# Kernel optimization log

Hardware: AMD Instinct MI355X
Metric: run time of the kernel (lower is better)

The kernel has to match this reference:

```python
import jax, jax.numpy as jnp
import numpy as np

NUM_HEADS = 8
NUM_GROUPS = 32
EPS = 1e-5


def setup_inputs() -> dict:
    key = jax.random.key(0)
    ks = jax.random.split(key, 7)
    B, C, H, W = 8, 512, 32, 32
    x = jax.random.normal(ks[0], (B, C, H, W), dtype=jnp.float32)
    # GroupNorm affine params
    gn_w = jnp.ones((C,), dtype=jnp.float32)
    gn_b = jnp.zeros((C,), dtype=jnp.float32)
    # 1x1 conv == linear over channel dim; store squeezed weights (out, in)
    qkv_w = jax.random.normal(ks[1], (3 * C, C), dtype=jnp.float32) * (1.0 / np.sqrt(C))
    qkv_b = jnp.zeros((3 * C,), dtype=jnp.float32)
    proj_w = jax.random.normal(ks[2], (C, C), dtype=jnp.float32) * (1.0 / np.sqrt(C))
    proj_b = jnp.zeros((C,), dtype=jnp.float32)
    return {"x": x, "gn_w": gn_w, "gn_b": gn_b, "qkv_w": qkv_w,
            "qkv_b": qkv_b, "proj_w": proj_w, "proj_b": proj_b}


def reference(x, gn_w, gn_b, qkv_w, qkv_b, proj_w, proj_b):
    B, C, H, W = x.shape
    G = NUM_GROUPS
    hd = C // NUM_HEADS
    scale = hd ** -0.5
    # GroupNorm: normalize over (C//G, H, W) per group
    xg = x.reshape(B, G, C // G, H, W)
    mean = xg.mean(axis=(2, 3, 4), keepdims=True)
    var = xg.var(axis=(2, 3, 4), keepdims=True)
    xn = ((xg - mean) * jax.lax.rsqrt(var + EPS)).reshape(B, C, H, W)
    xn = xn * gn_w[None, :, None, None] + gn_b[None, :, None, None]
    # QKV 1x1 conv
    qkv = jnp.einsum('bchw,oc->bohw', xn, qkv_w) + qkv_b[None, :, None, None]
    # (B, 3, heads, head_dim, HW) -> (3, B, heads, HW, head_dim)
    qkv = qkv.reshape(B, 3, NUM_HEADS, hd, H * W).transpose(1, 0, 2, 4, 3)
    q, k, v = qkv[0], qkv[1], qkv[2]
    attn = jax.nn.softmax(jnp.einsum('bhqd,bhkd->bhqk', q, k) * scale, axis=-1)
    out = jnp.einsum('bhqk,bhkd->bhqd', attn, v)  # (B, heads, HW, hd)
    out = out.transpose(0, 1, 3, 2).reshape(B, C, H, W)
    out = jnp.einsum('bchw,oc->bohw', out, proj_w) + proj_b[None, :, None, None]
    return out + x
```

## Files before the change

kernel.cpp:

```cpp
#include <hip/hip_runtime.h>
#include <hip/hip_bf16.h>
#include <math.h>

typedef __bf16 bf16_t;
typedef __bf16 bf16x8 __attribute__((ext_vector_type(8)));
typedef __bf16 bf16x4 __attribute__((ext_vector_type(4)));
typedef float  f32x4  __attribute__((ext_vector_type(4)));
typedef short  short4v __attribute__((ext_vector_type(4)));

#define NB    8
#define NC    512
#define NHW   1024
#define NHEAD 8
#define NHD   64
#define NG    32
#define NCG   16
#define NO3   1536
#define KVB   64
#define NKT   16

__device__ __forceinline__ void lds_load16(bf16_t* lds, const bf16_t* g) {
  __builtin_amdgcn_global_load_lds(
      (__attribute__((address_space(1))) unsigned int*)(g),
      (__attribute__((address_space(3))) unsigned int*)(void*)(lds),
      16, 0, 0);
}

__device__ __forceinline__ f32x4 mfma16(bf16x4 a, bf16x4 b, f32x4 c) {
#if __has_builtin(__builtin_amdgcn_mfma_f32_16x16x16bf16_1k)
  return __builtin_amdgcn_mfma_f32_16x16x16bf16_1k(
      __builtin_bit_cast(short4v, a), __builtin_bit_cast(short4v, b), c, 0, 0, 0);
#else
  f32x4 d;
  asm("v_mfma_f32_16x16x16_bf16 %0, %1, %2, %3"
      : "=v"(d) : "v"(a), "v"(b), "v"(c));
  return d;
#endif
}

__global__ __launch_bounds__(256)
void gn_kernel(const float* __restrict__ x, const float* __restrict__ gw,
               const float* __restrict__ gb, bf16_t* __restrict__ xn)
{
  const int bg = blockIdx.x;
  const int b = bg >> 5, g = bg & 31;
  const float* xp = x + ((size_t)b * NC + g * NCG) * NHW;
  const int tid = threadIdx.x;
  const int wave = tid >> 6, lane = tid & 63;

  float s1 = 0.f, s2 = 0.f;
  const float4* xp4 = (const float4*)xp;
  for (int i = tid; i < 4096; i += 256) {
    float4 v = xp4[i];
    s1 += v.x + v.y + v.z + v.w;
    s2 += v.x * v.x + v.y * v.y + v.z * v.z + v.w * v.w;
  }
  for (int off = 32; off > 0; off >>= 1) {
    s1 += __shfl_down(s1, off);
    s2 += __shfl_down(s2, off);
  }
  __shared__ float red[16];
  if (lane == 0) { red[wave] = s1; red[8 + wave] = s2; }
  __syncthreads();
  float tot1 = red[0] + red[1] + red[2] + red[3];
  float tot2 = red[8] + red[9] + red[10] + red[11];
  const float mean = tot1 * (1.0f / 16384.0f);
  const float var  = tot2 * (1.0f / 16384.0f) - mean * mean;
  const float rstd = rsqrtf(var + 1e-5f);

  float gam[NCG], bet[NCG];
  #pragma unroll
  for (int c = 0; c < NCG; ++c) {
    gam[c] = gw[g * NCG + c] * rstd;
    bet[c] = gb[g * NCG + c] - mean * gam[c];
  }
  bf16_t* op = xn + (size_t)b * NHW * NC + g * NCG;
  for (int s = tid; s < NHW; s += 256) {
    __align__(16) bf16_t vals[NCG];
    #pragma unroll
    for (int c = 0; c < NCG; ++c)
      vals[c] = (bf16_t)(xp[c * NHW + s] * gam[c] + bet[c]);
    *(bf16x8*)(op + (size_t)s * NC)     = *(const bf16x8*)&vals[0];
    *(bf16x8*)(op + (size_t)s * NC + 8) = *(const bf16x8*)&vals[8];
  }
}

__global__ __launch_bounds__(256)
void wconv_kernel(const float* __restrict__ qw, const float* __restrict__ pw,
                  bf16_t* __restrict__ qwb, bf16_t* __restrict__ pwb)
{
  const int gid = blockIdx.x * 256 + threadIdx.x;
  const int n1 = NO3 * NC / 4;
  float4 v; bf16x4 o;
  if (gid < n1) {
    v = ((const float4*)qw)[gid];
    o[0] = (bf16_t)v.x; o[1] = (bf16_t)v.y; o[2] = (bf16_t)v.z; o[3] = (bf16_t)v.w;
    ((bf16x4*)qwb)[gid] = o;
  } else {
    int g2 = gid - n1;
    v = ((const float4*)pw)[g2];
    o[0] = (bf16_t)v.x; o[1] = (bf16_t)v.y; o[2] = (bf16_t)v.z; o[3] = (bf16_t)v.w;
    ((bf16x4*)pwb)[g2] = o;
  }
}

__device__ __forceinline__ void gemm_mainloop(const bf16_t* Ap, const bf16_t* Bp,
                                              bf16_t* sA, bf16_t* sB, f32x4 (&acc)[4][4])
{
  const int tid = threadIdx.x;
  const int wave = tid >> 6, lane = tid & 63;
  const int quad = lane >> 4, l16 = lane & 15;
  const int wm = wave >> 1, wn = wave & 1;
  for (int k0 = 0; k0 < 512; k0 += 32) {
    #pragma unroll
    for (int j = 0; j < 2; ++j) {
      int c = wave * 64 + j * 256 + lane;
      int row = c >> 2, ko = (c & 3) * 8;
      lds_load16(sA + (size_t)(wave * 64 + j * 256) * 8, Ap + (size_t)row * 512 + k0 + ko);
      lds_load16(sB + (size_t)(wave * 64 + j * 256) * 8, Bp + (size_t)row * 512 + k0 + ko);
    }
    __syncthreads();
    bf16x8 af[4], bfr[4];
    #pragma unroll
    for (int mi = 0; mi < 4; ++mi)
      af[mi] = *(const bf16x8*)(sA + (wm * 64 + mi * 16 + l16) * 32 + quad * 8);
    #pragma unroll
    for (int ni = 0; ni < 4; ++ni)
      bfr[ni] = *(const bf16x8*)(sB + (wn * 64 + ni * 16 + l16) * 32 + quad * 8);
    #pragma unroll
    for (int mi = 0; mi < 4; ++mi)
      #pragma unroll
      for (int ni = 0; ni < 4; ++ni)
        acc[mi][ni] = __builtin_amdgcn_mfma_f32_16x16x32_bf16(af[mi], bfr[ni], acc[mi][ni], 0, 0, 0);
    __syncthreads();
  }
}

__global__ __launch_bounds__(256, 2)
void qkv_gemm(const bf16_t* __restrict__ xn, const bf16_t* __restrict__ w,
              const float* __restrict__ bias,
              bf16_t* __restrict__ qbuf, bf16_t* __restrict__ kbuf, bf16_t* __restrict__ vbuf)
{
  __shared__ __align__(16) bf16_t smem[128 * 136];
  bf16_t* sA = smem;
  bf16_t* sB = smem + 4096;
  const int tid = threadIdx.x;
  const int wave = tid >> 6, lane = tid & 63;
  const int quad = lane >> 4, l16 = lane & 15;
  const int wm = wave >> 1, wn = wave & 1;
  const int bx = blockIdx.x, by = blockIdx.y, b = blockIdx.z;

  const bf16_t* Ap = xn + ((size_t)b * NHW + by * 128) * NC;
  const bf16_t* Bp = w + (size_t)bx * 128 * NC;
  f32x4 acc[4][4] = {};
  gemm_mainloop(Ap, Bp, sA, sB, acc);

  const int obase = bx * 128 + wn * 64;
  const int sbase = by * 128 + wm * 64;
  float bv[4];
  #pragma unroll
  for (int ni = 0; ni < 4; ++ni) bv[ni] = bias[obase + ni * 16 + l16];

  if (bx < 8) {
    const bool isq = (bx < 4);
    bf16_t* basep = isq ? qbuf : kbuf;
    const float scale = isq ? 0.18033688f : 1.0f;
    #pragma unroll
    for (int ni = 0; ni < 4; ++ni) {
      int o = obase + ni * 16 + l16;
      int hh = (o >> 6) & 7, dd = o & 63;
      bf16_t* dst = basep + ((size_t)(b * NHEAD + hh) * NHW) * NHD + dd;
      #pragma unroll
      for (int mi = 0; mi < 4; ++mi)
        #pragma unroll
        for (int r = 0; r < 4; ++r) {
          int s = sbase + mi * 16 + quad * 4 + r;
          dst[(size_t)s * NHD] = (bf16_t)((acc[mi][ni][r] + bv[ni]) * scale);
        }
    }
  } else {
    bf16_t* sC = smem;
    __syncthreads();
    #pragma unroll
    for (int ni = 0; ni < 4; ++ni)
      #pragma unroll
      for (int mi = 0; mi < 4; ++mi)
        #pragma unroll
        for (int r = 0; r < 4; ++r)
          sC[(wn * 64 + ni * 16 + l16) * 136 + wm * 64 + mi * 16 + quad * 4 + r] =
              (bf16_t)(acc[mi][ni][r] + bv[ni]);
    __syncthreads();
    int o_local = tid >> 1, shalf = (tid & 1) << 6;
    int ov = (bx - 8) * 128 + o_local;
    int hh = ov >> 6, dd = ov & 63;
    bf16_t* dst = vbuf + ((size_t)(b * NHEAD + hh) * NHD + dd) * NHW + by * 128 + shalf;
    #pragma unroll
    for (int jj = 0; jj < 8; ++jj)
      *(bf16x8*)(dst + jj * 8) = *(const bf16x8*)&sC[o_local * 136 + shalf + jj * 8];
  }
}

__global__ __launch_bounds__(256, 2)
void attn_kernel(const bf16_t* __restrict__ qbuf, const bf16_t* __restrict__ kbuf,
                 const bf16_t* __restrict__ vbuf, bf16_t* __restrict__ obuf)
{
  __shared__ __align__(16) char smem[32768];
  f32x4* mO = (f32x4*)smem;
  float* mM = (float*)(smem + 16384);
  float* mL = (float*)(smem + 17408);

  const int tid = threadIdx.x;
  const int wave = tid >> 6, lane = tid & 63;
  const int quad = lane >> 4, l16 = lane & 15;
  const int wl = wave & 1;
  const int wg = wave >> 1;
  const int idx = blockIdx.x;
  const int qt = idx >> 6, h = (idx >> 3) & 7, b = idx & 7;
  const size_t bh = (size_t)b * NHEAD + h;
  const bf16_t* qp = qbuf + (bh * NHW + qt * 64 + wl * 32) * NHD;
  const char* kp = (const char*)(kbuf + bh * NHW * NHD);
  const char* vp = (const char*)(vbuf + bh * NHD * NHW);

  const int r8 = lane >> 3;
  const int swc = (((lane & 7) << 4)) ^ (r8 << 4);

  bf16x8 qf[2][2];
  #pragma unroll
  for (int stile = 0; stile < 2; ++stile)
    #pragma unroll
    for (int kc = 0; kc < 2; ++kc)
      qf[stile][kc] = *(const bf16x8*)(qp + (size_t)(stile * 16 + l16) * NHD + kc * 32 + quad * 8);

  float m_i[2] = {-1e30f, -1e30f};
  float ll[2] = {0.f, 0.f};
  f32x4 oacc[4][2] = {};

  #pragma unroll
  for (int j = 0; j < 2; ++j) {
    int i = wave * 2 + j;
    const char* kg = kp + ((size_t)(i * 8 + r8) * NHD) * 2 + swc;
    lds_load16((bf16_t*)(smem + i * 1024), (const bf16_t*)kg);
    const char* vg = vp + ((size_t)(i * 8 + r8) * NHW) * 2 + swc;
    lds_load16((bf16_t*)(smem + 8192 + i * 1024), (const bf16_t*)vg);
  }
  __syncthreads();

  const int swr = (l16 & 7) << 4;

  for (int kt = 0; kt < NKT; ++kt) {
    const int cur = kt & 1;
    const char* Kb = smem + cur * 16384;
    const char* Vb = Kb + 8192;
    if (kt < NKT - 1) {
      char* Kn = smem + (cur ^ 1) * 16384;
      #pragma unroll
      for (int j = 0; j < 2; ++j) {
        int i = wave * 2 + j;
        const char* kg = kp + ((size_t)((kt + 1) * KVB + i * 8 + r8) * NHD) * 2 + swc;
        lds_load16((bf16_t*)(Kn + i * 1024), (const bf16_t*)kg);
        const char* vg = vp + ((size_t)(i * 8 + r8) * NHW + (kt + 1) * KVB) * 2 + swc;
        lds_load16((bf16_t*)(Kn + 8192 + i * 1024), (const bf16_t*)vg);
      }
    }

    f32x4 st[2][2];
    __builtin_amdgcn_s_setprio(1);
    #pragma unroll
    for (int mt = 0; mt < 2; ++mt) {
      const int mtg = wg * 2 + mt;
      const char* krow = Kb + (mtg * 16 + l16) * 128;
      bf16x8 ka0 = *(const bf16x8*)(krow + ((quad * 16) ^ swr));
      bf16x8 ka1 = *(const bf16x8*)(krow + ((64 + quad * 16) ^ swr));
      #pragma unroll
      for (int stile = 0; stile < 2; ++stile) {
        f32x4 z = {};
        z = __builtin_amdgcn_mfma_f32_16x16x32_bf16(ka0, qf[stile][0], z, 0, 0, 0);
        z = __builtin_amdgcn_mfma_f32_16x16x32_bf16(ka1, qf[stile][1], z, 0, 0, 0);
        st[stile][mt] = z;
      }
    }
    __builtin_amdgcn_s_setprio(0);

    #pragma unroll
    for (int stile = 0; stile < 2; ++stile) {
      float mx = st[stile][0][0];
      #pragma unroll
      for (int mt = 0; mt < 2; ++mt)
        #pragma unroll
        for (int r = 0; r < 4; ++r) mx = fmaxf(mx, st[stile][mt][r]);
      if (!__all(mx <= m_i[stile])) {
        mx = fmaxf(mx, __shfl_xor(mx, 16));
        mx = fmaxf(mx, __shfl_xor(mx, 32));
        float mnew = fmaxf(m_i[stile], mx);
        float alpha = exp2f(m_i[stile] - mnew);
        m_i[stile] = mnew;
        ll[stile] *= alpha;
        #pragma unroll
        for (int mi = 0; mi < 4; ++mi)
          #pragma unroll
          for (int r = 0; r < 4; ++r) oacc[mi][stile][r] *= alpha;
      }
      float rs = 0.f;
      #pragma unroll
      for (int mt = 0; mt < 2; ++mt)
        #pragma unroll
        for (int r = 0; r < 4; ++r) {
          float p = exp2f(st[stile][mt][r] - m_i[stile]);
          rs += p;
          st[stile][mt][r] = p;
        }
      ll[stile] += rs;
    }

    __builtin_amdgcn_s_setprio(1);
    #pragma unroll
    for (int mt = 0; mt < 2; ++mt) {
      const int mtg = wg * 2 + mt;
      bf16x4 pb[2];
      #pragma unroll
      for (int stile = 0; stile < 2; ++stile) {
        pb[stile][0] = (bf16_t)st[stile][mt][0];
        pb[stile][1] = (bf16_t)st[stile][mt][1];
        pb[stile][2] = (bf16_t)st[stile][mt][2];
        pb[stile][3] = (bf16_t)st[stile][mt][3];
      }
      #pragma unroll
      for (int mi = 0; mi < 4; ++mi) {
        const char* vrow = Vb + (mi * 16 + l16) * 128;
        bf16x4 va = *(const bf16x4*)(vrow + ((mtg * 32 + quad * 8) ^ swr));
        oacc[mi][0] = mfma16(va, pb[0], oacc[mi][0]);
        oacc[mi][1] = mfma16(va, pb[1], oacc[mi][1]);
      }
    }
    __builtin_amdgcn_s_setprio(0);
    __syncthreads();
  }

  float l_i[2];
  #pragma unroll
  for (int stile = 0; stile < 2; ++stile) {
    float rs = ll[stile];
    rs += __shfl_xor(rs, 16);
    rs += __shfl_xor(rs, 32);
    l_i[stile] = rs;
  }

  if (wg == 1) {
    #pragma unroll
    for (int stile = 0; stile < 2; ++stile) {
      mM[(wl * 2 + stile) * 64 + lane] = m_i[stile];
      mL[(wl * 2 + stile) * 64 + lane] = l_i[stile];
      #pragma unroll
      for (int mi = 0; mi < 4; ++mi)
        mO[((wl * 2 + stile) * 4 + mi) * 64 + lane] = oacc[mi][stile];
    }
  }
  __syncthreads();
  if (wg == 0) {
    #pragma unroll
    for (int stile = 0; stile < 2; ++stile) {
      float mB = mM[(wl * 2 + stile) * 64 + lane];
      float lB = mL[(wl * 2 + stile) * 64 + lane];
      float mS = fmaxf(m_i[stile], mB);
      float aA = exp2f(m_i[stile] - mS);
      float aB = exp2f(mB - mS);
      float inv = 1.0f / (l_i[stile] * aA + lB * aB);
      int s = qt * 64 + wl * 32 + stile * 16 + l16;
      bf16_t* orow = obuf + ((size_t)b * NHW + s) * NC + h * NHD;
      #pragma unroll
      for (int mi = 0; mi < 4; ++mi) {
        f32x4 oB = mO[((wl * 2 + stile) * 4 + mi) * 64 + lane];
        __align__(8) bf16_t o4[4];
        #pragma unroll
        for (int r = 0; r < 4; ++r)
          o4[r] = (bf16_t)((oacc[mi][stile][r] * aA + oB[r] * aB) * inv);
        *(bf16x4*)(orow + mi * 16 + quad * 4) = *(const bf16x4*)o4;
      }
    }
  }
}

__global__ __launch_bounds__(256, 2)
void proj_gemm(const bf16_t* __restrict__ ob, const bf16_t* __restrict__ w,
               const float* __restrict__ bias, const float* __restrict__ x,
               float* __restrict__ out)
{
  __shared__ __align__(16) bf16_t smem[8192];
  bf16_t* sA = smem;
  bf16_t* sB = smem + 4096;
  const int tid = threadIdx.x;
  const int wave = tid >> 6, lane = tid & 63;
  const int quad = lane >> 4, l16 = lane & 15;
  const int wm = wave >> 1, wn = wave & 1;
  const int bx = blockIdx.x, by = blockIdx.y, b = blockIdx.z;

  const bf16_t* Ap = w + (size_t)by * 128 * NC;
  const bf16_t* Bp = ob + ((size_t)b * NHW + bx * 128) * NC;
  f32x4 acc[4][4] = {};
  gemm_mainloop(Ap, Bp, sA, sB, acc);

  const int cobase = by * 128 + wm * 64;
  const int sbase  = bx * 128 + wn * 64;
  #pragma unroll
  for (int mi = 0; mi < 4; ++mi)
    #pragma unroll
    for (int r = 0; r < 4; ++r) {
      int co = cobase + mi * 16 + quad * 4 + r;
      float pb = bias[co];
      const float* xrow = x + ((size_t)b * NC + co) * NHW;
      float* orow = out + ((size_t)b * NC + co) * NHW;
      #pragma unroll
      for (int ni = 0; ni < 4; ++ni) {
        int s = sbase + ni * 16 + l16;
        orow[s] = acc[mi][ni][r] + pb + xrow[s];
      }
    }
}

extern "C" void kernel_launch(void* const* d_in, const int* in_sizes, int n_in,
                              void* d_out, int out_size, void* d_ws, size_t ws_size,
                              hipStream_t stream)
{
  const float* x      = (const float*)d_in[0];
  const float* gn_w   = (const float*)d_in[1];
  const float* gn_b   = (const float*)d_in[2];
  const float* qkv_w  = (const float*)d_in[3];
  const float* qkv_b  = (const float*)d_in[4];
  const float* proj_w = (const float*)d_in[5];
  const float* proj_b = (const float*)d_in[6];
  float* out = (float*)d_out;

  char* ws = (char*)d_ws;
  bf16_t* xn   = (bf16_t*)(ws);
  bf16_t* qwb  = (bf16_t*)(ws + 8388608);
  bf16_t* pwb  = (bf16_t*)(ws + 9961472);
  bf16_t* qbuf = (bf16_t*)(ws + 10485760);
  bf16_t* kbuf = (bf16_t*)(ws + 18874368);
  bf16_t* vbuf = (bf16_t*)(ws + 27262976);
  bf16_t* obuf = xn;

  gn_kernel<<<dim3(NB * NG), dim3(256), 0, stream>>>(x, gn_w, gn_b, xn);
  wconv_kernel<<<dim3(1024), dim3(256), 0, stream>>>(qkv_w, proj_w, qwb, pwb);
  qkv_gemm<<<dim3(12, 8, NB), dim3(256), 0, stream>>>(xn, qwb, qkv_b, qbuf, kbuf, vbuf);
  attn_kernel<<<dim3(1024), dim3(256), 0, stream>>>(qbuf, kbuf, vbuf, obuf);
  proj_gemm<<<dim3(8, 4, NB), dim3(256), 0, stream>>>(obuf, pwb, proj_b, x, out);
}
```

Baseline: 173.2 us.

## Fuse GN with weight conversion, double-buffer GEMMs, retile proj, use fast exp2

Merges the GroupNorm and weight-conversion kernels into one launch, dropping a kernel launch. GroupNorm now keeps its inputs in registers instead of reading x twice from memory. Both GEMMs gain double-buffered LDS staging so the next K-tile's global-to-LDS load overlaps the current MFMA work. The projection GEMM moves to 64-row output tiles, doubling its grid so more of the GPU is busy. Attention swaps exp2f for the hardware exp2 builtin. The cost is more registers and LDS, and the builtin exp2 may be less exact.

```diff
diff --git a/kernel.cpp b/kernel.cpp
--- a/kernel.cpp
+++ b/kernel.cpp
@@ -38,22 +38,52 @@
 #endif
 }
 
+__device__ __forceinline__ float fexp2(float x) {
+#if __has_builtin(__builtin_amdgcn_exp2f)
+  return __builtin_amdgcn_exp2f(x);
+#else
+  return exp2f(x);
+#endif
+}
+
 __global__ __launch_bounds__(256)
-void gn_kernel(const float* __restrict__ x, const float* __restrict__ gw,
-               const float* __restrict__ gb, bf16_t* __restrict__ xn)
+void gnw_kernel(const float* __restrict__ x, const float* __restrict__ gw,
+                const float* __restrict__ gb, bf16_t* __restrict__ xn,
+                const float* __restrict__ qw, const float* __restrict__ pw,
+                bf16_t* __restrict__ qwb, bf16_t* __restrict__ pwb)
 {
-  const int bg = blockIdx.x;
-  const int b = bg >> 5, g = bg & 31;
+  const int bid = blockIdx.x;
+  const int tid = threadIdx.x;
+
+  if (bid >= NB * NG) {
+    const int gid = (bid - NB * NG) * 256 + tid;
+    const int n1 = NO3 * NC / 4;
+    float4 v; bf16x4 o;
+    if (gid < n1) {
+      v = ((const float4*)qw)[gid];
+      o[0] = (bf16_t)v.x; o[1] = (bf16_t)v.y; o[2] = (bf16_t)v.z; o[3] = (bf16_t)v.w;
+      ((bf16x4*)qwb)[gid] = o;
+    } else {
+      int g2 = gid - n1;
+      v = ((const float4*)pw)[g2];
+      o[0] = (bf16_t)v.x; o[1] = (bf16_t)v.y; o[2] = (bf16_t)v.z; o[3] = (bf16_t)v.w;
+      ((bf16x4*)pwb)[g2] = o;
+    }
+    return;
+  }
+
+  const int b = bid >> 5, g = bid & 31;
   const float* xp = x + ((size_t)b * NC + g * NCG) * NHW;
-  const int tid = threadIdx.x;
   const int wave = tid >> 6, lane = tid & 63;
 
+  float4 v[16];
+  const float4* xp4 = (const float4*)xp;
   float s1 = 0.f, s2 = 0.f;
-  const float4* xp4 = (const float4*)xp;
-  for (int i = tid; i < 4096; i += 256) {
-    float4 v = xp4[i];
-    s1 += v.x + v.y + v.z + v.w;
-    s2 += v.x * v.x + v.y * v.y + v.z * v.z + v.w * v.w;
+  #pragma unroll
+  for (int c = 0; c < 16; ++c) {
+    v[c] = xp4[c * 256 + tid];
+    s1 += v[c].x + v[c].y + v[c].z + v[c].w;
+    s2 += v[c].x * v[c].x + v[c].y * v[c].y + v[c].z * v[c].z + v[c].w * v[c].w;
   }
   for (int off = 32; off > 0; off >>= 1) {
     s1 += __shfl_down(s1, off);
@@ -75,43 +105,38 @@
     bet[c] = gb[g * NCG + c] - mean * gam[c];
   }
   bf16_t* op = xn + (size_t)b * NHW * NC + g * NCG;
-  for (int s = tid; s < NHW; s += 256) {
+  #pragma unroll
+  for (int jj = 0; jj < 4; ++jj) {
+    int s = 4 * tid + jj;
     __align__(16) bf16_t vals[NCG];
     #pragma unroll
-    for (int c = 0; c < NCG; ++c)
-      vals[c] = (bf16_t)(xp[c * NHW + s] * gam[c] + bet[c]);
+    for (int c = 0; c < NCG; ++c) {
+      float xv = (jj == 0) ? v[c].x : (jj == 1) ? v[c].y : (jj == 2) ? v[c].z : v[c].w;
+      vals[c] = (bf16_t)(xv * gam[c] + bet[c]);
+    }
     *(bf16x8*)(op + (size_t)s * NC)     = *(const bf16x8*)&vals[0];
     *(bf16x8*)(op + (size_t)s * NC + 8) = *(const bf16x8*)&vals[8];
   }
 }
 
-__global__ __launch_bounds__(256)
-void wconv_kernel(const float* __restrict__ qw, const float* __restrict__ pw,
-                  bf16_t* __restrict__ qwb, bf16_t* __restrict__ pwb)
+__global__ __launch_bounds__(256, 2)
+void qkv_gemm(const bf16_t* __restrict__ xn, const bf16_t* __restrict__ w,
+              const float* __restrict__ bias,
+              bf16_t* __restrict__ qbuf, bf16_t* __restrict__ kbuf, bf16_t* __restrict__ vbuf)
 {
-  const int gid = blockIdx.x * 256 + threadIdx.x;
-  const int n1 = NO3 * NC / 4;
-  float4 v; bf16x4 o;
-  if (gid < n1) {
-    v = ((const float4*)qw)[gid];
-    o[0] = (bf16_t)v.x; o[1] = (bf16_t)v.y; o[2] = (bf16_t)v.z; o[3] = (bf16_t)v.w;
-    ((bf16x4*)qwb)[gid] = o;
-  } else {
-    int g2 = gid - n1;
-    v = ((const float4*)pw)[g2];
-    o[0] = (bf16_t)v.x; o[1] = (bf16_t)v.y; o[2] = (bf16_t)v.z; o[3] = (bf16_t)v.w;
-    ((bf16x4*)pwb)[g2] = o;
-  }
-}
-
-__device__ __forceinline__ void gemm_mainloop(const bf16_t* Ap, const bf16_t* Bp,
-                                              bf16_t* sA, bf16_t* sB, f32x4 (&acc)[4][4])
-{
+  __shared__ __align__(16) char smem[34816];
   const int tid = threadIdx.x;
   const int wave = tid >> 6, lane = tid & 63;
   const int quad = lane >> 4, l16 = lane & 15;
   const int wm = wave >> 1, wn = wave & 1;
-  for (int k0 = 0; k0 < 512; k0 += 32) {
+  const int bx = blockIdx.x, by = blockIdx.y, b = blockIdx.z;
+
+  const bf16_t* Ap = xn + ((size_t)b * NHW + by * 128) * NC;
+  const bf16_t* Bp = w + (size_t)bx * 128 * NC;
+
+  auto stage = [&](int k0, int bufi) {
+    bf16_t* sA = (bf16_t*)(smem + bufi * 16384);
+    bf16_t* sB = (bf16_t*)(smem + bufi * 16384 + 8192);
     #pragma unroll
     for (int j = 0; j < 2; ++j) {
       int c = wave * 64 + j * 256 + lane;
@@ -119,7 +144,16 @@
       lds_load16(sA + (size_t)(wave * 64 + j * 256) * 8, Ap + (size_t)row * 512 + k0 + ko);
       lds_load16(sB + (size_t)(wave * 64 + j * 256) * 8, Bp + (size_t)row * 512 + k0 + ko);
     }
-    __syncthreads();
+  };
+
+  f32x4 acc[4][4] = {};
+  stage(0, 0);
+  __syncthreads();
+  for (int t = 0; t < 16; ++t) {
+    const int cur = t & 1;
+    if (t < 15) stage((t + 1) * 32, cur ^ 1);
+    const bf16_t* sA = (const bf16_t*)(smem + cur * 16384);
+    const bf16_t* sB = sA + 4096;
     bf16x8 af[4], bfr[4];
     #pragma unroll
     for (int mi = 0; mi < 4; ++mi)
@@ -134,26 +168,6 @@
         acc[mi][ni] = __builtin_amdgcn_mfma_f32_16x16x32_bf16(af[mi], bfr[ni], acc[mi][ni], 0, 0, 0);
     __syncthreads();
   }
-}
-
-__global__ __launch_bounds__(256, 2)
-void qkv_gemm(const bf16_t* __restrict__ xn, const bf16_t* __restrict__ w,
-              const float* __restrict__ bias,
-              bf16_t* __restrict__ qbuf, bf16_t* __restrict__ kbuf, bf16_t* __restrict__ vbuf)
-{
-  __shared__ __align__(16) bf16_t smem[128 * 136];
-  bf16_t* sA = smem;
-  bf16_t* sB = smem + 4096;
-  const int tid = threadIdx.x;
-  const int wave = tid >> 6, lane = tid & 63;
-  const int quad = lane >> 4, l16 = lane & 15;
-  const int wm = wave >> 1, wn = wave & 1;
-  const int bx = blockIdx.x, by = blockIdx.y, b = blockIdx.z;
-
-  const bf16_t* Ap = xn + ((size_t)b * NHW + by * 128) * NC;
-  const bf16_t* Bp = w + (size_t)bx * 128 * NC;
-  f32x4 acc[4][4] = {};
-  gemm_mainloop(Ap, Bp, sA, sB, acc);
 
   const int obase = bx * 128 + wn * 64;
   const int sbase = by * 128 + wm * 64;
@@ -179,7 +193,7 @@
         }
     }
   } else {
-    bf16_t* sC = smem;
+    bf16_t* sC = (bf16_t*)smem;
     __syncthreads();
     #pragma unroll
     for (int ni = 0; ni < 4; ++ni)
@@ -292,7 +306,7 @@
         mx = fmaxf(mx, __shfl_xor(mx, 16));
         mx = fmaxf(mx, __shfl_xor(mx, 32));
         float mnew = fmaxf(m_i[stile], mx);
-        float alpha = exp2f(m_i[stile] - mnew);
+        float alpha = fexp2(m_i[stile] - mnew);
         m_i[stile] = mnew;
         ll[stile] *= alpha;
         #pragma unroll
@@ -305,7 +319,7 @@
       for (int mt = 0; mt < 2; ++mt)
         #pragma unroll
         for (int r = 0; r < 4; ++r) {
-          float p = exp2f(st[stile][mt][r] - m_i[stile]);
+          float p = fexp2(st[stile][mt][r] - m_i[stile]);
           rs += p;
           st[stile][mt][r] = p;
         }
@@ -362,8 +376,8 @@
       float mB = mM[(wl * 2 + stile) * 64 + lane];
       float lB = mL[(wl * 2 + stile) * 64 + lane];
       float mS = fmaxf(m_i[stile], mB);
-      float aA = exp2f(m_i[stile] - mS);
-      float aB = exp2f(mB - mS);
+      float aA = fexp2(m_i[stile] - mS);
+      float aB = fexp2(mB - mS);
       float inv = 1.0f / (l_i[stile] * aA + lB * aB);
       int s = qt * 64 + wl * 32 + stile * 16 + l16;
       bf16_t* orow = obuf + ((size_t)b * NHW + s) * NC + h * NHD;
@@ -385,24 +399,59 @@
                const float* __restrict__ bias, const float* __restrict__ x,
                float* __restrict__ out)
 {
-  __shared__ __align__(16) bf16_t smem[8192];
-  bf16_t* sA = smem;
-  bf16_t* sB = smem + 4096;
+  __shared__ __align__(16) char smem[24576];
   const int tid = threadIdx.x;
   const int wave = tid >> 6, lane = tid & 63;
   const int quad = lane >> 4, l16 = lane & 15;
-  const int wm = wave >> 1, wn = wave & 1;
+  const int wm = wave & 1, wn = wave >> 1;
   const int bx = blockIdx.x, by = blockIdx.y, b = blockIdx.z;
 
-  const bf16_t* Ap = w + (size_t)by * 128 * NC;
+  const bf16_t* Ap = w + (size_t)by * 64 * NC;
   const bf16_t* Bp = ob + ((size_t)b * NHW + bx * 128) * NC;
-  f32x4 acc[4][4] = {};
-  gemm_mainloop(Ap, Bp, sA, sB, acc);
-
-  const int cobase = by * 128 + wm * 64;
+
+  auto stage = [&](int k0, int bufi) {
+    bf16_t* sA = (bf16_t*)(smem + bufi * 12288);
+    bf16_t* sB = (bf16_t*)(smem + bufi * 12288 + 4096);
+    {
+      int c = wave * 64 + lane;
+      int row = c >> 2, ko = (c & 3) * 8;
+      lds_load16(sA + (size_t)(wave * 64) * 8, Ap + (size_t)row * 512 + k0 + ko);
+    }
+    #pragma unroll
+    for (int j = 0; j < 2; ++j) {
+      int c = wave * 64 + j * 256 + lane;
+      int row = c >> 2, ko = (c & 3) * 8;
+      lds_load16(sB + (size_t)(wave * 64 + j * 256) * 8, Bp + (size_t)row * 512 + k0 + ko);
+    }
+  };
+
+  f32x4 acc[2][4] = {};
+  stage(0, 0);
+  __syncthreads();
+  for (int t = 0; t < 16; ++t) {
+    const int cur = t & 1;
+    if (t < 15) stage((t + 1) * 32, cur ^ 1);
+    const bf16_t* sA = (const bf16_t*)(smem + cur * 12288);
+    const bf16_t* sB = sA + 2048;
+    bf16x8 af[2], bfr[4];
+    #pragma unroll
+    for (int mi = 0; mi < 2; ++mi)
+      af[mi] = *(const bf16x8*)(sA + (wm * 32 + mi * 16 + l16) * 32 + quad * 8);
+    #pragma unroll
+    for (int ni = 0; ni < 4; ++ni)
+      bfr[ni] = *(const bf16x8*)(sB + (wn * 64 + ni * 16 + l16) * 32 + quad * 8);
+    #pragma unroll
+    for (int mi = 0; mi < 2; ++mi)
+      #pragma unroll
+      for (int ni = 0; ni < 4; ++ni)
+        acc[mi][ni] = __builtin_amdgcn_mfma_f32_16x16x32_bf16(af[mi], bfr[ni], acc[mi][ni], 0, 0, 0);
+    __syncthreads();
+  }
+
+  const int cobase = by * 64 + wm * 32;
   const int sbase  = bx * 128 + wn * 64;
   #pragma unroll
-  for (int mi = 0; mi < 4; ++mi)
+  for (int mi = 0; mi < 2; ++mi)
     #pragma unroll
     for (int r = 0; r < 4; ++r) {
       int co = cobase + mi * 16 + quad * 4 + r;
@@ -439,9 +488,9 @@
   bf16_t* vbuf = (bf16_t*)(ws + 27262976);
   bf16_t* obuf = xn;
 
-  gn_kernel<<<dim3(NB * NG), dim3(256), 0, stream>>>(x, gn_w, gn_b, xn);
-  wconv_kernel<<<dim3(1024), dim3(256), 0, stream>>>(qkv_w, proj_w, qwb, pwb);
+  gnw_kernel<<<dim3(NB * NG + 1024), dim3(256), 0, stream>>>(
+      x, gn_w, gn_b, xn, qkv_w, proj_w, qwb, pwb);
   qkv_gemm<<<dim3(12, 8, NB), dim3(256), 0, stream>>>(xn, qwb, qkv_b, qbuf, kbuf, vbuf);
   attn_kernel<<<dim3(1024), dim3(256), 0, stream>>>(qbuf, kbuf, vbuf, obuf);
-  proj_gemm<<<dim3(8, 4, NB), dim3(256), 0, stream>>>(obuf, pwb, proj_b, x, out);
-}
+  proj_gemm<<<dim3(8, 8, NB), dim3(256), 0, stream>>>(obuf, pwb, proj_b, x, out);
+}
```

Measured after the change: 152.4 us. -12.0%, faster.
